# Optimization experiments

Measured on AMD Instinct MI355X. Metric: run time of the kernel, lower is better.

The kernel has to match this reference:

```python
import jax, jax.numpy as jnp
import numpy as np

# (multiplicity, l) segments, ir_mul layout: each segment stored as (2l+1, mul)
IRREPS = [(256, 0), (256, 1), (256, 2), (256, 3)]
BATCH = 8192
DIM = sum(m * (2 * l + 1) for m, l in IRREPS)  # 4096


def _real_basis_U(l):
    """Unitary change of basis from complex to real spherical harmonics (degree l)."""
    n = 2 * l + 1
    U = np.zeros((n, n), dtype=np.complex128)
    U[l, l] = 1.0
    s = 1.0 / np.sqrt(2.0)
    for mu in range(1, l + 1):
        U[l + mu, l - mu] = s
        U[l + mu, l + mu] = s * (-1.0) ** mu
        U[l - mu, l - mu] = 1j * s
        U[l - mu, l + mu] = -1j * s * (-1.0) ** mu
    return U


def _x_generator_eig(l):
    """Eigendecomposition (constants) of the x-axis angular-momentum operator in the real basis."""
    m = np.arange(-l, l + 1)
    n = 2 * l + 1
    Jp = np.zeros((n, n), dtype=np.complex128)
    mm = m[:-1]
    Jp[np.arange(1, n), np.arange(0, n - 1)] = np.sqrt(l * (l + 1) - mm * (mm + 1))
    Jx = (Jp + Jp.conj().T) / 2.0
    U = _real_basis_U(l)
    Jx_r = U @ Jx @ U.conj().T  # Hermitian
    w, V = np.linalg.eigh(Jx_r)  # w = -l..l (integers), V unitary
    return w, V


def _y_rotation(theta, l):
    """Rotation about y in the real irrep basis, built directly from the angle
    encoding [cos(l t),...,cos(t),1,sin(t),...,sin(l t)] -- diag cos(m t), antidiag +/- sin(m t)."""
    B = theta.shape[0]
    n = 2 * l + 1
    mu = jnp.arange(1, l + 1, dtype=theta.dtype)
    c = jnp.cos(mu * theta[:, None])  # [B, l]
    s = jnp.sin(mu * theta[:, None])  # [B, l]
    one = jnp.ones((B, 1), theta.dtype)
    zero = jnp.zeros((B, 1), theta.dtype)
    diag = jnp.concatenate([c[:, ::-1], one, c], axis=-1)    # [B, n]
    anti = jnp.concatenate([-s[:, ::-1], zero, s], axis=-1)  # [B, n]
    idx = jnp.arange(n)
    R = jnp.zeros((B, n, n), theta.dtype)
    R = R.at[:, idx, idx].set(diag)
    R = R.at[:, idx, idx[::-1]].add(anti)
    return R


def _x_rotation(theta, l, dtype):
    """Rotation about x: X(t) = Re(V diag(exp(-i t w)) V^H), done in real arithmetic."""
    w, V = _x_generator_eig(l)
    w = jnp.asarray(w, dtype)
    Vr = jnp.asarray(np.ascontiguousarray(V.real), dtype)
    Vi = jnp.asarray(np.ascontiguousarray(V.imag), dtype)
    C = jnp.cos(theta[:, None] * w)  # [B, n]
    S = jnp.sin(theta[:, None] * w)  # [B, n]
    X = (jnp.einsum('ik,bk,jk->bij', Vr, C, Vr)
         + jnp.einsum('ik,bk,jk->bij', Vi, C, Vi)
         + jnp.einsum('ik,bk,jk->bij', Vi, S, Vr)
         - jnp.einsum('ik,bk,jk->bij', Vr, S, Vi))
    return X


def _rotate(gamma, beta, alpha, x):
    # yxy Euler rotation: first gamma about y, then beta about x, then alpha about y.
    outs = []
    off = 0
    for mul, l in IRREPS:
        n = 2 * l + 1
        seg = x[:, off:off + n * mul].reshape(-1, n, mul)  # ir_mul layout
        D = _y_rotation(alpha, l) @ _x_rotation(beta, l, x.dtype) @ _y_rotation(gamma, l)
        outs.append(jnp.einsum('bij,bjm->bim', D, seg).reshape(-1, n * mul))
        off += n * mul
    return jnp.concatenate(outs, axis=-1)


def setup_inputs() -> dict:
    key = jax.random.key(0)
    kg, kb, ka, kx = jax.random.split(key, 4)
    return {
        'gamma': jax.random.normal(kg, (BATCH,), jnp.float32),
        'beta': jax.random.normal(kb, (BATCH,), jnp.float32),
        'alpha': jax.random.normal(ka, (BATCH,), jnp.float32),
        'x': jax.random.normal(kx, (BATCH, DIM), jnp.float32),
    }


def reference(gamma, beta, alpha, x):
    return _rotate(gamma, beta, alpha, x)
```

## Files before the change

### kernel.cpp

```cpp
#include <hip/hip_runtime.h>
#include <math.h>

#define BATCH 8192
#define DIM 4096


struct FT { float v[495]; };

constexpr double csqrt(double x) {
  double g = x > 1.0 ? x : 1.0;
  for (int i = 0; i < 50; ++i) g = 0.5 * (g + x / g);
  return g;
}

constexpr void mmc(int n, const double* A, const double* B, double* C) {
  for (int i = 0; i < n; ++i)
    for (int j = 0; j < n; ++j) {
      double s = 0.0;
      for (int k = 0; k < n; ++k) s += A[i * n + k] * B[k * n + j];
      C[i * n + j] = s;
    }
}

constexpr FT compute_ft() {
  FT o{};
  for (int l = 1; l <= 3; ++l) {
    const int n = 2 * l + 1, nn = n * n;
    double JX[49] = {}, UR[49] = {}, UI[49] = {};
    for (int a = 0; a < n - 1; ++a) {
      double m = (double)(a - l);
      double v = 0.5 * csqrt((double)(l * (l + 1)) - m * (m + 1.0));
      JX[(a + 1) * n + a] = v;
      JX[a * n + (a + 1)] = v;
    }
    UR[l * n + l] = 1.0;
    const double s = csqrt(0.5);
    for (int mu = 1; mu <= l; ++mu) {
      double sg = (mu & 1) ? -1.0 : 1.0;
      UR[(l + mu) * n + (l - mu)] = s;
      UR[(l + mu) * n + (l + mu)] = s * sg;
      UI[(l - mu) * n + (l - mu)] = s;
      UI[(l - mu) * n + (l + mu)] = -s * sg;
    }
    double MR[49] = {}, MI[49] = {};
    mmc(n, UR, JX, MR);
    mmc(n, UI, JX, MI);
    double K[49] = {};
    for (int a = 0; a < n; ++a)
      for (int b = 0; b < n; ++b) {
        double acc = 0.0;
        for (int c = 0; c < n; ++c)
          acc += MI[a * n + c] * UR[b * n + c] - MR[a * n + c] * UI[b * n + c];
        K[a * n + b] = acc;
      }
    const double TH = 0.78539816339744830962;
    double S[49] = {}, P[49] = {}, T[49] = {};
    for (int i = 0; i < nn; ++i) S[i] = K[i] * (TH / 16.0);
    for (int i = 0; i < n; ++i) P[i * n + i] = 1.0;
    for (int t = 12; t >= 1; --t) {
      mmc(n, S, P, T);
      double inv = 1.0 / (double)t;
      for (int i = 0; i < nn; ++i) P[i] = T[i] * inv;
      for (int i = 0; i < n; ++i) P[i * n + i] += 1.0;
    }
    for (int q = 0; q < 4; ++q) {
      mmc(n, P, P, T);
      for (int i = 0; i < nn; ++i) P[i] = T[i];
    }
    double acc[7][49] = {};
    double Ek[49] = {}, Et[49] = {};
    for (int i = 0; i < n; ++i) Ek[i * n + i] = 1.0;
    const double r2 = csqrt(0.5);
    const double c8[8] = {1.0, r2, 0.0, -r2, -1.0, -r2, 0.0, r2};
    const double s8[8] = {0.0, r2, 1.0, r2, 0.0, -r2, -1.0, -r2};
    for (int k = 0; k < 8; ++k) {
      for (int i = 0; i < nn; ++i) acc[0][i] += 0.125 * Ek[i];
      for (int mu = 1; mu <= l; ++mu) {
        int a8 = (mu * k) & 7;
        double cc = 0.25 * c8[a8], ss = 0.25 * s8[a8];
        for (int i = 0; i < nn; ++i) {
          acc[2 * mu - 1][i] += cc * Ek[i];
          acc[2 * mu][i] += ss * Ek[i];
        }
      }
      mmc(n, Ek, P, Et);
      for (int i = 0; i < nn; ++i) Ek[i] = Et[i];
    }
    int base = (l == 1) ? 0 : ((l == 2) ? 27 : 152);
    for (int t = 0; t <= 2 * l; ++t)
      for (int i = 0; i < nn; ++i) o.v[base + t * nn + i] = (float)acc[t][i];
  }
  return o;
}

__device__ __constant__ FT c_tb = compute_ft();

typedef float vf4 __attribute__((ext_vector_type(4)));


__device__ __forceinline__ vf4 vfma4(float a, vf4 v, vf4 acc) {
  return acc + a * v;
}

__global__ __launch_bounds__(256) void rot_apply(
    const float* __restrict__ gamma, const float* __restrict__ beta,
    const float* __restrict__ alpha, const float* __restrict__ x,
    float* __restrict__ out) {
  __shared__ float Dl[4][83];
  const int tid = threadIdx.x;
  const int b0 = blockIdx.x * 4;

  for (int e = tid; e < 332; e += 256) {
    int row = e / 83;
    int idx = e - row * 83;
    int l, n, basec, r;
    if (idx < 9)       { l = 1; n = 3; basec = 0;   r = idx; }
    else if (idx < 34) { l = 2; n = 5; basec = 27;  r = idx - 9; }
    else               { l = 3; n = 7; basec = 152; r = idx - 34; }
    int i = r / n, j = r - i * n;
    int b = b0 + row;
    float al = alpha[b], be = beta[b], ga = gamma[b];

    float cb1, sb1;
    sincosf(be, &sb1, &cb1);
    float cb2 = cb1 * cb1 - sb1 * sb1, sb2 = 2.f * sb1 * cb1;
    float cb3 = cb2 * cb1 - sb2 * sb1, sb3 = sb2 * cb1 + cb2 * sb1;
    float cb[4] = {1.f, cb1, cb2, cb3};
    float sb[4] = {0.f, sb1, sb2, sb3};

    const float* C = c_tb.v + basec;
    int ip = n - 1 - i, jp = n - 1 - j;
    float xij = 0.f, xijp = 0.f, xipj = 0.f, xipjp = 0.f;
    for (int tt = 0; tt <= 2 * l; ++tt) {
      float coef = (tt == 0) ? 1.f : ((tt & 1) ? cb[(tt + 1) >> 1] : sb[tt >> 1]);
      const float* M = C + tt * n * n;
      xij   = fmaf(coef, M[i * n + j],   xij);
      xijp  = fmaf(coef, M[i * n + jp],  xijp);
      xipj  = fmaf(coef, M[ip * n + j],  xipj);
      xipjp = fmaf(coef, M[ip * n + jp], xipjp);
    }
    float sa, ca, sg, cg;
    sincosf((float)(i - l) * al, &sa, &ca);
    sincosf((float)(j - l) * ga, &sg, &cg);
    Dl[row][idx] = (ca * xij + sa * xipj) * cg - (ca * xijp + sa * xipjp) * sg;
  }
  __syncthreads();

  const int lane = tid & 63;
  const int row = tid >> 6;
  const size_t b = (size_t)(b0 + row);
  const vf4* __restrict__ xin = (const vf4*)x + b * 1024;
  vf4* __restrict__ xo = (vf4*)out + b * 1024;
  const float* D = Dl[row];

  vf4 v0 = xin[lane];
  vf4 v1[3], v2[5], v3[7];
  #pragma unroll
  for (int j = 0; j < 3; ++j) v1[j] = xin[64 + j * 64 + lane];
  #pragma unroll
  for (int j = 0; j < 5; ++j) v2[j] = xin[256 + j * 64 + lane];
  #pragma unroll
  for (int j = 0; j < 7; ++j) v3[j] = xin[576 + j * 64 + lane];

  __builtin_nontemporal_store(v0, &xo[lane]);

  #pragma unroll
  for (int i = 0; i < 3; ++i) {
    vf4 o = (vf4)(0.f);
    #pragma unroll
    for (int j = 0; j < 3; ++j) o = vfma4(D[i * 3 + j], v1[j], o);
    __builtin_nontemporal_store(o, &xo[64 + i * 64 + lane]);
  }

  #pragma unroll
  for (int i = 0; i < 5; ++i) {
    vf4 o = (vf4)(0.f);
    #pragma unroll
    for (int j = 0; j < 5; ++j) o = vfma4(D[9 + i * 5 + j], v2[j], o);
    __builtin_nontemporal_store(o, &xo[256 + i * 64 + lane]);
  }

  #pragma unroll
  for (int i = 0; i < 7; ++i) {
    vf4 o = (vf4)(0.f);
    #pragma unroll
    for (int j = 0; j < 7; ++j) o = vfma4(D[34 + i * 7 + j], v3[j], o);
    __builtin_nontemporal_store(o, &xo[576 + i * 64 + lane]);
  }
}

extern "C" void kernel_launch(void* const* d_in, const int* in_sizes, int n_in,
                              void* d_out, int out_size, void* d_ws, size_t ws_size,
                              hipStream_t stream) {
  const float* gamma = (const float*)d_in[0];
  const float* beta  = (const float*)d_in[1];
  const float* alpha = (const float*)d_in[2];
  const float* x     = (const float*)d_in[3];
  float* out = (float*)d_out;

  rot_apply<<<BATCH / 4, 256, 0, stream>>>(gamma, beta, alpha, x, out);
}
```

Measured before the change: 49.10 us.

## Split Wigner-D construction into separate kernel and stream x with early loads

Moves the per-batch rotation matrix construction into a separate build_D kernel that writes D to workspace, then a streaming kernel loads x before reading D from workspace, so global loads overlap the D fetch instead of waiting on trig work. Angle tables now use multiple-angle recurrences instead of per-entry sincos. It adds a kernel launch and a workspace round trip of about 2.7MB, and build_D runs with only 32 blocks, one thread per batch, which serializes 83 entries per thread. A fused fallback is kept if the workspace is too small.

```diff
diff --git a/kernel.cpp b/kernel.cpp
--- a/kernel.cpp
+++ b/kernel.cpp
@@ -3,6 +3,7 @@
 
 #define BATCH 8192
 #define DIM 4096
+#define DSTRIDE 83
 
 
 struct FT { float v[495]; };
@@ -97,52 +98,142 @@
 
 typedef float vf4 __attribute__((ext_vector_type(4)));
 
-
-__device__ __forceinline__ vf4 vfma4(float a, vf4 v, vf4 acc) {
-  return acc + a * v;
-}
-
-__global__ __launch_bounds__(256) void rot_apply(
+__device__ __forceinline__ vf4 vfma4(float a, vf4 v, vf4 acc) { return acc + a * v; }
+
+__device__ __forceinline__ float d_entry(int l, int n, int basec, int i, int j,
+                                         const float* cb, const float* sb,
+                                         const float* ca, const float* sa,
+                                         const float* cg, const float* sg) {
+  const float* C = c_tb.v + basec;
+  int ip = n - 1 - i, jp = n - 1 - j;
+  float xij = 0.f, xijp = 0.f, xipj = 0.f, xipjp = 0.f;
+  for (int tt = 0; tt <= 2 * l; ++tt) {
+    float coef = (tt == 0) ? 1.f : ((tt & 1) ? cb[(tt + 1) >> 1] : sb[tt >> 1]);
+    const float* M = C + tt * n * n;
+    xij   = fmaf(coef, M[i * n + j],   xij);
+    xijp  = fmaf(coef, M[i * n + jp],  xijp);
+    xipj  = fmaf(coef, M[ip * n + j],  xipj);
+    xipjp = fmaf(coef, M[ip * n + jp], xipjp);
+  }
+  int di = i - l, dj = j - l;
+  float cai = ca[di < 0 ? -di : di];
+  float sai = di < 0 ? -sa[-di] : sa[di];
+  float cgj = cg[dj < 0 ? -dj : dj];
+  float sgj = dj < 0 ? -sg[-dj] : sg[dj];
+  return (cai * xij + sai * xipj) * cgj - (cai * xijp + sai * xipjp) * sgj;
+}
+
+__device__ __forceinline__ void angle_tables(float t, float* c, float* s) {
+  c[0] = 1.f; s[0] = 0.f;
+  sincosf(t, &s[1], &c[1]);
+  c[2] = c[1] * c[1] - s[1] * s[1];
+  s[2] = 2.f * s[1] * c[1];
+  c[3] = c[2] * c[1] - s[2] * s[1];
+  s[3] = s[2] * c[1] + c[2] * s[1];
+}
+
+__global__ __launch_bounds__(256) void build_D(
+    const float* __restrict__ gamma, const float* __restrict__ beta,
+    const float* __restrict__ alpha, float* __restrict__ Dws) {
+  int b = blockIdx.x * 256 + threadIdx.x;
+  if (b >= BATCH) return;
+  float cb[4], sb[4], ca[4], sa[4], cg[4], sg[4];
+  angle_tables(beta[b], cb, sb);
+  angle_tables(alpha[b], ca, sa);
+  angle_tables(gamma[b], cg, sg);
+  float* Drow = Dws + (size_t)b * DSTRIDE;
+  int baseD = 0;
+  #pragma unroll
+  for (int l = 1; l <= 3; ++l) {
+    int n = 2 * l + 1;
+    int basec = (l == 1) ? 0 : ((l == 2) ? 27 : 152);
+    for (int i = 0; i < n; ++i)
+      for (int j = 0; j < n; ++j)
+        Drow[baseD + i * n + j] =
+            d_entry(l, n, basec, i, j, cb, sb, ca, sa, cg, sg);
+    baseD += n * n;
+  }
+}
+
+__global__ __launch_bounds__(256, 4) void rot_stream(
+    const float* __restrict__ Dws, const float* __restrict__ x,
+    float* __restrict__ out) {
+  __shared__ float Dl[4 * DSTRIDE];
+  const int tid = threadIdx.x;
+  const int b0 = blockIdx.x * 4;
+  const int lane = tid & 63;
+  const int row = tid >> 6;
+  const size_t b = (size_t)(b0 + row);
+  const vf4* __restrict__ xin = (const vf4*)x + b * 1024;
+  vf4* __restrict__ xo = (vf4*)out + b * 1024;
+
+  vf4 v0 = xin[lane];
+  vf4 v1[3], v2[5], v3[7];
+  #pragma unroll
+  for (int j = 0; j < 3; ++j) v1[j] = xin[64 + j * 64 + lane];
+  #pragma unroll
+  for (int j = 0; j < 5; ++j) v2[j] = xin[256 + j * 64 + lane];
+  #pragma unroll
+  for (int j = 0; j < 7; ++j) v3[j] = xin[576 + j * 64 + lane];
+
+  for (int e = tid; e < 4 * DSTRIDE; e += 256)
+    Dl[e] = Dws[(size_t)b0 * DSTRIDE + e];
+  __syncthreads();
+
+  asm volatile("" ::"v"(v0), "v"(v1[0]), "v"(v1[1]), "v"(v1[2]), "v"(v2[0]),
+               "v"(v2[1]), "v"(v2[2]), "v"(v2[3]), "v"(v2[4]), "v"(v3[0]),
+               "v"(v3[1]), "v"(v3[2]), "v"(v3[3]), "v"(v3[4]), "v"(v3[5]),
+               "v"(v3[6]));
+
+  const float* D = Dl + row * DSTRIDE;
+
+  __builtin_nontemporal_store(v0, &xo[lane]);
+
+  #pragma unroll
+  for (int i = 0; i < 3; ++i) {
+    vf4 o = (vf4)(0.f);
+    #pragma unroll
+    for (int j = 0; j < 3; ++j) o = vfma4(D[i * 3 + j], v1[j], o);
+    __builtin_nontemporal_store(o, &xo[64 + i * 64 + lane]);
+  }
+  #pragma unroll
+  for (int i = 0; i < 5; ++i) {
+    vf4 o = (vf4)(0.f);
+    #pragma unroll
+    for (int j = 0; j < 5; ++j) o = vfma4(D[9 + i * 5 + j], v2[j], o);
+    __builtin_nontemporal_store(o, &xo[256 + i * 64 + lane]);
+  }
+  #pragma unroll
+  for (int i = 0; i < 7; ++i) {
+    vf4 o = (vf4)(0.f);
+    #pragma unroll
+    for (int j = 0; j < 7; ++j) o = vfma4(D[34 + i * 7 + j], v3[j], o);
+    __builtin_nontemporal_store(o, &xo[576 + i * 64 + lane]);
+  }
+}
+
+__global__ __launch_bounds__(256) void rot_fused(
     const float* __restrict__ gamma, const float* __restrict__ beta,
     const float* __restrict__ alpha, const float* __restrict__ x,
     float* __restrict__ out) {
-  __shared__ float Dl[4][83];
+  __shared__ float Dl[4][DSTRIDE];
   const int tid = threadIdx.x;
   const int b0 = blockIdx.x * 4;
 
-  for (int e = tid; e < 332; e += 256) {
-    int row = e / 83;
-    int idx = e - row * 83;
+  for (int e = tid; e < 4 * DSTRIDE; e += 256) {
+    int row = e / DSTRIDE;
+    int idx = e - row * DSTRIDE;
     int l, n, basec, r;
     if (idx < 9)       { l = 1; n = 3; basec = 0;   r = idx; }
     else if (idx < 34) { l = 2; n = 5; basec = 27;  r = idx - 9; }
     else               { l = 3; n = 7; basec = 152; r = idx - 34; }
     int i = r / n, j = r - i * n;
     int b = b0 + row;
-    float al = alpha[b], be = beta[b], ga = gamma[b];
-
-    float cb1, sb1;
-    sincosf(be, &sb1, &cb1);
-    float cb2 = cb1 * cb1 - sb1 * sb1, sb2 = 2.f * sb1 * cb1;
-    float cb3 = cb2 * cb1 - sb2 * sb1, sb3 = sb2 * cb1 + cb2 * sb1;
-    float cb[4] = {1.f, cb1, cb2, cb3};
-    float sb[4] = {0.f, sb1, sb2, sb3};
-
-    const float* C = c_tb.v + basec;
-    int ip = n - 1 - i, jp = n - 1 - j;
-    float xij = 0.f, xijp = 0.f, xipj = 0.f, xipjp = 0.f;
-    for (int tt = 0; tt <= 2 * l; ++tt) {
-      float coef = (tt == 0) ? 1.f : ((tt & 1) ? cb[(tt + 1) >> 1] : sb[tt >> 1]);
-      const float* M = C + tt * n * n;
-      xij   = fmaf(coef, M[i * n + j],   xij);
-      xijp  = fmaf(coef, M[i * n + jp],  xijp);
-      xipj  = fmaf(coef, M[ip * n + j],  xipj);
-      xipjp = fmaf(coef, M[ip * n + jp], xipjp);
-    }
-    float sa, ca, sg, cg;
-    sincosf((float)(i - l) * al, &sa, &ca);
-    sincosf((float)(j - l) * ga, &sg, &cg);
-    Dl[row][idx] = (ca * xij + sa * xipj) * cg - (ca * xijp + sa * xipjp) * sg;
+    float cb[4], sb[4], ca[4], sa[4], cg[4], sg[4];
+    angle_tables(beta[b], cb, sb);
+    angle_tables(alpha[b], ca, sa);
+    angle_tables(gamma[b], cg, sg);
+    Dl[row][idx] = d_entry(l, n, basec, i, j, cb, sb, ca, sa, cg, sg);
   }
   __syncthreads();
 
@@ -163,7 +254,6 @@
   for (int j = 0; j < 7; ++j) v3[j] = xin[576 + j * 64 + lane];
 
   __builtin_nontemporal_store(v0, &xo[lane]);
-
   #pragma unroll
   for (int i = 0; i < 3; ++i) {
     vf4 o = (vf4)(0.f);
@@ -171,7 +261,6 @@
     for (int j = 0; j < 3; ++j) o = vfma4(D[i * 3 + j], v1[j], o);
     __builtin_nontemporal_store(o, &xo[64 + i * 64 + lane]);
   }
-
   #pragma unroll
   for (int i = 0; i < 5; ++i) {
     vf4 o = (vf4)(0.f);
@@ -179,7 +268,6 @@
     for (int j = 0; j < 5; ++j) o = vfma4(D[9 + i * 5 + j], v2[j], o);
     __builtin_nontemporal_store(o, &xo[256 + i * 64 + lane]);
   }
-
   #pragma unroll
   for (int i = 0; i < 7; ++i) {
     vf4 o = (vf4)(0.f);
@@ -198,5 +286,12 @@
   const float* x     = (const float*)d_in[3];
   float* out = (float*)d_out;
 
-  rot_apply<<<BATCH / 4, 256, 0, stream>>>(gamma, beta, alpha, x, out);
-}
+  const size_t need = (size_t)BATCH * DSTRIDE * sizeof(float);
+  if (ws_size >= need) {
+    float* Dws = (float*)d_ws;
+    build_D<<<BATCH / 256, 256, 0, stream>>>(gamma, beta, alpha, Dws);
+    rot_stream<<<BATCH / 4, 256, 0, stream>>>(Dws, x, out);
+  } else {
+    rot_fused<<<BATCH / 4, 256, 0, stream>>>(gamma, beta, alpha, x, out);
+  }
+}
```

After: 61.69 us. 1.26x slower.

## Use grid-stride persistent blocks and issue x loads before computing D

Applied to the files above, without the earlier changes.

Replaces the one-block-per-4-rows launch with a fixed grid of 512 blocks that loop over row groups, double-buffering the shared D matrices. Each iteration issues the global loads of x before computing the rotation matrices, so memory latency overlaps with the trig and coefficient math. An asm barrier keeps the loads from being sunk past the compute. The per-entry sincos of multiples of alpha and gamma is replaced by angle-addition tables. The trade-off is fewer resident blocks and more registers held live across the D computation.

```diff
diff --git a/kernel.cpp b/kernel.cpp
--- a/kernel.cpp
+++ b/kernel.cpp
@@ -3,6 +3,9 @@
 
 #define BATCH 8192
 #define DIM 4096
+#define DSTRIDE 83
+#define DPAD 96
+#define GRID 512
 
 
 struct FT { float v[495]; };
@@ -97,95 +100,110 @@
 
 typedef float vf4 __attribute__((ext_vector_type(4)));
 
-
-__device__ __forceinline__ vf4 vfma4(float a, vf4 v, vf4 acc) {
-  return acc + a * v;
-}
-
-__global__ __launch_bounds__(256) void rot_apply(
+__device__ __forceinline__ vf4 vfma4(float a, vf4 v, vf4 acc) { return acc + a * v; }
+
+__device__ __forceinline__ float d_entry(int l, int n, int basec, int i, int j,
+                                         const float* cb, const float* sb,
+                                         const float* ca, const float* sa,
+                                         const float* cg, const float* sg) {
+  const float* C = c_tb.v + basec;
+  int ip = n - 1 - i, jp = n - 1 - j;
+  float xij = 0.f, xijp = 0.f, xipj = 0.f, xipjp = 0.f;
+  for (int tt = 0; tt <= 2 * l; ++tt) {
+    float coef = (tt == 0) ? 1.f : ((tt & 1) ? cb[(tt + 1) >> 1] : sb[tt >> 1]);
+    const float* M = C + tt * n * n;
+    xij   = fmaf(coef, M[i * n + j],   xij);
+    xijp  = fmaf(coef, M[i * n + jp],  xijp);
+    xipj  = fmaf(coef, M[ip * n + j],  xipj);
+    xipjp = fmaf(coef, M[ip * n + jp], xipjp);
+  }
+  int di = i - l, dj = j - l;
+  float cai = ca[di < 0 ? -di : di];
+  float sai = di < 0 ? -sa[-di] : sa[di];
+  float cgj = cg[dj < 0 ? -dj : dj];
+  float sgj = dj < 0 ? -sg[-dj] : sg[dj];
+  return (cai * xij + sai * xipj) * cgj - (cai * xijp + sai * xipjp) * sgj;
+}
+
+__device__ __forceinline__ void angle_tables(float t, float* c, float* s) {
+  c[0] = 1.f; s[0] = 0.f;
+  sincosf(t, &s[1], &c[1]);
+  c[2] = c[1] * c[1] - s[1] * s[1];
+  s[2] = 2.f * s[1] * c[1];
+  c[3] = c[2] * c[1] - s[2] * s[1];
+  s[3] = s[2] * c[1] + c[2] * s[1];
+}
+
+__global__ __launch_bounds__(256) void rot_gs(
     const float* __restrict__ gamma, const float* __restrict__ beta,
     const float* __restrict__ alpha, const float* __restrict__ x,
     float* __restrict__ out) {
-  __shared__ float Dl[4][83];
+  __shared__ float Dl[2][4][DPAD];
   const int tid = threadIdx.x;
-  const int b0 = blockIdx.x * 4;
-
-  for (int e = tid; e < 332; e += 256) {
-    int row = e / 83;
-    int idx = e - row * 83;
-    int l, n, basec, r;
-    if (idx < 9)       { l = 1; n = 3; basec = 0;   r = idx; }
-    else if (idx < 34) { l = 2; n = 5; basec = 27;  r = idx - 9; }
-    else               { l = 3; n = 7; basec = 152; r = idx - 34; }
-    int i = r / n, j = r - i * n;
-    int b = b0 + row;
-    float al = alpha[b], be = beta[b], ga = gamma[b];
-
-    float cb1, sb1;
-    sincosf(be, &sb1, &cb1);
-    float cb2 = cb1 * cb1 - sb1 * sb1, sb2 = 2.f * sb1 * cb1;
-    float cb3 = cb2 * cb1 - sb2 * sb1, sb3 = sb2 * cb1 + cb2 * sb1;
-    float cb[4] = {1.f, cb1, cb2, cb3};
-    float sb[4] = {0.f, sb1, sb2, sb3};
-
-    const float* C = c_tb.v + basec;
-    int ip = n - 1 - i, jp = n - 1 - j;
-    float xij = 0.f, xijp = 0.f, xipj = 0.f, xipjp = 0.f;
-    for (int tt = 0; tt <= 2 * l; ++tt) {
-      float coef = (tt == 0) ? 1.f : ((tt & 1) ? cb[(tt + 1) >> 1] : sb[tt >> 1]);
-      const float* M = C + tt * n * n;
-      xij   = fmaf(coef, M[i * n + j],   xij);
-      xijp  = fmaf(coef, M[i * n + jp],  xijp);
-      xipj  = fmaf(coef, M[ip * n + j],  xipj);
-      xipjp = fmaf(coef, M[ip * n + jp], xipjp);
-    }
-    float sa, ca, sg, cg;
-    sincosf((float)(i - l) * al, &sa, &ca);
-    sincosf((float)(j - l) * ga, &sg, &cg);
-    Dl[row][idx] = (ca * xij + sa * xipj) * cg - (ca * xijp + sa * xipjp) * sg;
-  }
-  __syncthreads();
-
   const int lane = tid & 63;
-  const int row = tid >> 6;
-  const size_t b = (size_t)(b0 + row);
-  const vf4* __restrict__ xin = (const vf4*)x + b * 1024;
-  vf4* __restrict__ xo = (vf4*)out + b * 1024;
-  const float* D = Dl[row];
-
-  vf4 v0 = xin[lane];
-  vf4 v1[3], v2[5], v3[7];
-  #pragma unroll
-  for (int j = 0; j < 3; ++j) v1[j] = xin[64 + j * 64 + lane];
-  #pragma unroll
-  for (int j = 0; j < 5; ++j) v2[j] = xin[256 + j * 64 + lane];
-  #pragma unroll
-  for (int j = 0; j < 7; ++j) v3[j] = xin[576 + j * 64 + lane];
-
-  __builtin_nontemporal_store(v0, &xo[lane]);
-
-  #pragma unroll
-  for (int i = 0; i < 3; ++i) {
-    vf4 o = (vf4)(0.f);
-    #pragma unroll
-    for (int j = 0; j < 3; ++j) o = vfma4(D[i * 3 + j], v1[j], o);
-    __builtin_nontemporal_store(o, &xo[64 + i * 64 + lane]);
-  }
-
-  #pragma unroll
-  for (int i = 0; i < 5; ++i) {
-    vf4 o = (vf4)(0.f);
-    #pragma unroll
-    for (int j = 0; j < 5; ++j) o = vfma4(D[9 + i * 5 + j], v2[j], o);
-    __builtin_nontemporal_store(o, &xo[256 + i * 64 + lane]);
-  }
-
-  #pragma unroll
-  for (int i = 0; i < 7; ++i) {
-    vf4 o = (vf4)(0.f);
-    #pragma unroll
-    for (int j = 0; j < 7; ++j) o = vfma4(D[34 + i * 7 + j], v3[j], o);
-    __builtin_nontemporal_store(o, &xo[576 + i * 64 + lane]);
+  const int wv = tid >> 6;
+
+  int p = 0;
+  for (int g = blockIdx.x; g < BATCH / 4; g += GRID, p ^= 1) {
+    const int b0 = g * 4;
+    const size_t b = (size_t)(b0 + wv);
+    const vf4* __restrict__ xin = (const vf4*)x + b * 1024;
+    vf4* __restrict__ xo = (vf4*)out + b * 1024;
+
+    vf4 v0 = xin[lane];
+    vf4 v1[3], v2[5], v3[7];
+    #pragma unroll
+    for (int j = 0; j < 3; ++j) v1[j] = xin[64 + j * 64 + lane];
+    #pragma unroll
+    for (int j = 0; j < 5; ++j) v2[j] = xin[256 + j * 64 + lane];
+    #pragma unroll
+    for (int j = 0; j < 7; ++j) v3[j] = xin[576 + j * 64 + lane];
+    asm volatile("" ::"v"(v0), "v"(v1[0]), "v"(v1[1]), "v"(v1[2]), "v"(v2[0]),
+                 "v"(v2[1]), "v"(v2[2]), "v"(v2[3]), "v"(v2[4]), "v"(v3[0]),
+                 "v"(v3[1]), "v"(v3[2]), "v"(v3[3]), "v"(v3[4]), "v"(v3[5]),
+                 "v"(v3[6]));
+
+    for (int e = tid; e < 4 * DSTRIDE; e += 256) {
+      int row = e / DSTRIDE;
+      int idx = e - row * DSTRIDE;
+      int l, n, basec, r;
+      if (idx < 9)       { l = 1; n = 3; basec = 0;   r = idx; }
+      else if (idx < 34) { l = 2; n = 5; basec = 27;  r = idx - 9; }
+      else               { l = 3; n = 7; basec = 152; r = idx - 34; }
+      int i = r / n, j = r - i * n;
+      int bb = b0 + row;
+      float cb[4], sbv[4], ca[4], sav[4], cg[4], sgv[4];
+      angle_tables(beta[bb], cb, sbv);
+      angle_tables(alpha[bb], ca, sav);
+      angle_tables(gamma[bb], cg, sgv);
+      Dl[p][row][idx] = d_entry(l, n, basec, i, j, cb, sbv, ca, sav, cg, sgv);
+    }
+    __syncthreads();
+
+    const float* D = Dl[p][wv];
+
+    __builtin_nontemporal_store(v0, &xo[lane]);
+    #pragma unroll
+    for (int i = 0; i < 3; ++i) {
+      vf4 o = (vf4)(0.f);
+      #pragma unroll
+      for (int j = 0; j < 3; ++j) o = vfma4(D[i * 3 + j], v1[j], o);
+      __builtin_nontemporal_store(o, &xo[64 + i * 64 + lane]);
+    }
+    #pragma unroll
+    for (int i = 0; i < 5; ++i) {
+      vf4 o = (vf4)(0.f);
+      #pragma unroll
+      for (int j = 0; j < 5; ++j) o = vfma4(D[9 + i * 5 + j], v2[j], o);
+      __builtin_nontemporal_store(o, &xo[256 + i * 64 + lane]);
+    }
+    #pragma unroll
+    for (int i = 0; i < 7; ++i) {
+      vf4 o = (vf4)(0.f);
+      #pragma unroll
+      for (int j = 0; j < 7; ++j) o = vfma4(D[34 + i * 7 + j], v3[j], o);
+      __builtin_nontemporal_store(o, &xo[576 + i * 64 + lane]);
+    }
   }
 }
 
@@ -198,5 +216,5 @@
   const float* x     = (const float*)d_in[3];
   float* out = (float*)d_out;
 
-  rot_apply<<<BATCH / 4, 256, 0, stream>>>(gamma, beta, alpha, x, out);
-}
+  rot_gs<<<GRID, 256, 0, stream>>>(gamma, beta, alpha, x, out);
+}
```

Result: slower. 58.32 us (+18.8%).

## Compute rotation matrices per wave in registers and broadcast with readlane

Applied to the files above, without the earlier changes.

Each wave now computes its own 83 Wigner-D entries, two per lane, instead of a block-wide LDS build followed by __syncthreads. The entries are broadcast to the whole wave with readlane, so the shared memory and the barrier go away. The x loads are issued before the D computation and pinned with an empty asm so that memory latency overlaps the trig work. The cost is duplicated index logic per lane, extra scalar readlanes in the FMA loops, and higher register pressure.

```diff
diff --git a/kernel.cpp b/kernel.cpp
--- a/kernel.cpp
+++ b/kernel.cpp
@@ -97,61 +97,60 @@
 
 typedef float vf4 __attribute__((ext_vector_type(4)));
 
-
-__device__ __forceinline__ vf4 vfma4(float a, vf4 v, vf4 acc) {
-  return acc + a * v;
-}
-
-__global__ __launch_bounds__(256) void rot_apply(
-    const float* __restrict__ gamma, const float* __restrict__ beta,
-    const float* __restrict__ alpha, const float* __restrict__ x,
-    float* __restrict__ out) {
-  __shared__ float Dl[4][83];
-  const int tid = threadIdx.x;
-  const int b0 = blockIdx.x * 4;
-
-  for (int e = tid; e < 332; e += 256) {
-    int row = e / 83;
-    int idx = e - row * 83;
-    int l, n, basec, r;
-    if (idx < 9)       { l = 1; n = 3; basec = 0;   r = idx; }
-    else if (idx < 34) { l = 2; n = 5; basec = 27;  r = idx - 9; }
-    else               { l = 3; n = 7; basec = 152; r = idx - 34; }
-    int i = r / n, j = r - i * n;
-    int b = b0 + row;
-    float al = alpha[b], be = beta[b], ga = gamma[b];
-
-    float cb1, sb1;
-    sincosf(be, &sb1, &cb1);
-    float cb2 = cb1 * cb1 - sb1 * sb1, sb2 = 2.f * sb1 * cb1;
-    float cb3 = cb2 * cb1 - sb2 * sb1, sb3 = sb2 * cb1 + cb2 * sb1;
-    float cb[4] = {1.f, cb1, cb2, cb3};
-    float sb[4] = {0.f, sb1, sb2, sb3};
-
-    const float* C = c_tb.v + basec;
-    int ip = n - 1 - i, jp = n - 1 - j;
-    float xij = 0.f, xijp = 0.f, xipj = 0.f, xipjp = 0.f;
-    for (int tt = 0; tt <= 2 * l; ++tt) {
-      float coef = (tt == 0) ? 1.f : ((tt & 1) ? cb[(tt + 1) >> 1] : sb[tt >> 1]);
-      const float* M = C + tt * n * n;
+__device__ __forceinline__ vf4 vfma4(float a, vf4 v, vf4 acc) { return acc + a * v; }
+
+__device__ __forceinline__ float entry_for(int e, float cb1, float cb2, float cb3,
+                                           float sb1, float sb2, float sb3,
+                                           float al, float ga) {
+  int l, n, basec, i, j;
+  if (e < 9)       { l = 1; n = 3; basec = 0;   int r = e;      i = r / 3; j = r - i * 3; }
+  else if (e < 34) { l = 2; n = 5; basec = 27;  int r = e - 9;  i = r / 5; j = r - i * 5; }
+  else             { l = 3; n = 7; basec = 152; int r = e - 34; i = r / 7; j = r - i * 7; }
+
+  const float* C = c_tb.v + basec;
+  const int ip = n - 1 - i, jp = n - 1 - j;
+  const int nn = n * n;
+  float xij = 0.f, xijp = 0.f, xipj = 0.f, xipjp = 0.f;
+  #pragma unroll
+  for (int tt = 0; tt < 7; ++tt) {
+    if (tt <= 2 * l) {
+      float coef;
+      if (tt == 0) coef = 1.f;
+      else if (tt == 1) coef = cb1;
+      else if (tt == 2) coef = sb1;
+      else if (tt == 3) coef = cb2;
+      else if (tt == 4) coef = sb2;
+      else if (tt == 5) coef = cb3;
+      else coef = sb3;
+      const float* M = C + tt * nn;
       xij   = fmaf(coef, M[i * n + j],   xij);
       xijp  = fmaf(coef, M[i * n + jp],  xijp);
       xipj  = fmaf(coef, M[ip * n + j],  xipj);
       xipjp = fmaf(coef, M[ip * n + jp], xipjp);
     }
-    float sa, ca, sg, cg;
-    sincosf((float)(i - l) * al, &sa, &ca);
-    sincosf((float)(j - l) * ga, &sg, &cg);
-    Dl[row][idx] = (ca * xij + sa * xipj) * cg - (ca * xijp + sa * xipjp) * sg;
-  }
-  __syncthreads();
-
+  }
+  float sa, ca, sg, cg;
+  sincosf((float)(i - l) * al, &sa, &ca);
+  sincosf((float)(j - l) * ga, &sg, &cg);
+  return (ca * xij + sa * xipj) * cg - (ca * xijp + sa * xipjp) * sg;
+}
+
+__device__ __forceinline__ float dget(float d0, float d1, int e) {
+  float s = (e < 64) ? d0 : d1;
+  return __builtin_bit_cast(
+      float, __builtin_amdgcn_readlane(__builtin_bit_cast(int, s), e & 63));
+}
+
+__global__ __launch_bounds__(256) void rot_wave(
+    const float* __restrict__ gamma, const float* __restrict__ beta,
+    const float* __restrict__ alpha, const float* __restrict__ x,
+    float* __restrict__ out) {
+  const int tid = threadIdx.x;
   const int lane = tid & 63;
-  const int row = tid >> 6;
-  const size_t b = (size_t)(b0 + row);
+  const int wv = tid >> 6;
+  const size_t b = (size_t)blockIdx.x * 4 + wv;
   const vf4* __restrict__ xin = (const vf4*)x + b * 1024;
   vf4* __restrict__ xo = (vf4*)out + b * 1024;
-  const float* D = Dl[row];
 
   vf4 v0 = xin[lane];
   vf4 v1[3], v2[5], v3[7];
@@ -161,6 +160,21 @@
   for (int j = 0; j < 5; ++j) v2[j] = xin[256 + j * 64 + lane];
   #pragma unroll
   for (int j = 0; j < 7; ++j) v3[j] = xin[576 + j * 64 + lane];
+  asm volatile("" ::"v"(v0), "v"(v1[0]), "v"(v1[1]), "v"(v1[2]), "v"(v2[0]),
+               "v"(v2[1]), "v"(v2[2]), "v"(v2[3]), "v"(v2[4]), "v"(v3[0]),
+               "v"(v3[1]), "v"(v3[2]), "v"(v3[3]), "v"(v3[4]), "v"(v3[5]),
+               "v"(v3[6]));
+
+  const float al = alpha[b], bt = beta[b], ga = gamma[b];
+  float cb1, sb1;
+  sincosf(bt, &sb1, &cb1);
+  const float cb2 = cb1 * cb1 - sb1 * sb1, sb2 = 2.f * sb1 * cb1;
+  const float cb3 = cb2 * cb1 - sb2 * sb1, sb3 = sb2 * cb1 + cb2 * sb1;
+
+  const float d0 = entry_for(lane, cb1, cb2, cb3, sb1, sb2, sb3, al, ga);
+  int e2 = lane + 64;
+  if (e2 > 82) e2 = 82;
+  const float d1 = entry_for(e2, cb1, cb2, cb3, sb1, sb2, sb3, al, ga);
 
   __builtin_nontemporal_store(v0, &xo[lane]);
 
@@ -168,23 +182,21 @@
   for (int i = 0; i < 3; ++i) {
     vf4 o = (vf4)(0.f);
     #pragma unroll
-    for (int j = 0; j < 3; ++j) o = vfma4(D[i * 3 + j], v1[j], o);
+    for (int j = 0; j < 3; ++j) o = vfma4(dget(d0, d1, i * 3 + j), v1[j], o);
     __builtin_nontemporal_store(o, &xo[64 + i * 64 + lane]);
   }
-
   #pragma unroll
   for (int i = 0; i < 5; ++i) {
     vf4 o = (vf4)(0.f);
     #pragma unroll
-    for (int j = 0; j < 5; ++j) o = vfma4(D[9 + i * 5 + j], v2[j], o);
+    for (int j = 0; j < 5; ++j) o = vfma4(dget(d0, d1, 9 + i * 5 + j), v2[j], o);
     __builtin_nontemporal_store(o, &xo[256 + i * 64 + lane]);
   }
-
   #pragma unroll
   for (int i = 0; i < 7; ++i) {
     vf4 o = (vf4)(0.f);
     #pragma unroll
-    for (int j = 0; j < 7; ++j) o = vfma4(D[34 + i * 7 + j], v3[j], o);
+    for (int j = 0; j < 7; ++j) o = vfma4(dget(d0, d1, 34 + i * 7 + j), v3[j], o);
     __builtin_nontemporal_store(o, &xo[576 + i * 64 + lane]);
   }
 }
@@ -198,5 +210,5 @@
   const float* x     = (const float*)d_in[3];
   float* out = (float*)d_out;
 
-  rot_apply<<<BATCH / 4, 256, 0, stream>>>(gamma, beta, alpha, x, out);
-}
+  rot_wave<<<BATCH / 4, 256, 0, stream>>>(gamma, beta, alpha, x, out);
+}
```

Measured after the change: 49.38 us. About the same (+0.6%).
